# Kernel optimization log

Measured on AMD Instinct MI355X. Metric: run time of the kernel, lower is better.

Reference implementation:

```python
import jax, jax.numpy as jnp
import numpy as np

N = 8192       # batch size
BIT = 32       # hash code length
NCLASS = 100   # number of classes
ALPHA = 0.1    # config['alpha'] (quantization weight)
BEITA = 1.0    # config['beita'] (classification weight)
GAMMA = 0.1    # config['gamma'] (balancing weight)
P = 2          # config['p']


def setup_inputs() -> dict:
    key = jax.random.key(0)
    k1, k2, k3 = jax.random.split(key, 3)
    u = jax.random.normal(k1, (N, BIT), dtype=jnp.float32)
    Y = jax.random.normal(k2, (N, NCLASS), dtype=jnp.float32)
    labels = jax.random.randint(k3, (N,), 0, NCLASS)
    y = jax.nn.one_hot(labels, NCLASS, dtype=jnp.float32)  # one-hot targets
    return {"u": u, "Y": Y, "y": y}


def _hash_loss(u, y):
    n = u.shape[0]
    theta = (u @ u.T) * 0.5                       # [N, N]
    sim = (y @ y.T > 0).astype(u.dtype)           # [N, N] pairwise same-class
    # log(1 + exp(theta)) - Sim * theta  (logaddexp = stable same math)
    pair = jnp.logaddexp(0.0, theta) - sim * theta
    mask_pos = sim > 0
    s1 = sim.sum() - n                            # positives minus diagonal
    s0 = n * n - sim.sum()                        # negatives
    s0 = jnp.where(s0 == 0, 1.0, s0)
    s1 = jnp.where(s1 == 0, 1.0, s1)
    s = s0 + s1
    scale = jnp.where(mask_pos, s / s1, s / s0)
    pair = pair * scale
    # original subtracts diag of the *detached* rescaled matrix
    pair = pair - jax.lax.stop_gradient(jnp.diag(jnp.diag(pair)))
    count = n * (n - 1) / 2
    return pair.sum() / 2.0 / count


def reference(u, Y, y):
    likelihood_loss = _hash_loss(u, y)
    # CrossEntropyLoss with soft (one-hot float) targets
    logp = jax.nn.log_softmax(Y, axis=-1)
    classification_loss = -(y * logp).sum(axis=-1).mean()
    m = u.mean(axis=1)
    if P == 1:
        quantization_loss = ALPHA * jnp.abs(m).mean()
    else:
        quantization_loss = ALPHA * (m ** 2).mean()
    b = jnp.sign(u)
    balancing_loss = GAMMA * ((u - b) ** 2).mean()
    return likelihood_loss + BEITA * classification_loss + quantization_loss + balancing_loss
```

## Files before the change

kernel.cpp:

```cpp
#include <hip/hip_runtime.h>
#include <math.h>
#include <type_traits>

#define N 8192
#define BIT 32
#define NCLASS 100
#define ALPHA 0.1
#define BEITA 1.0
#define GAMMA 0.1

#define BT 128
#define NT (N / BT)
#define NPAIRBLK (NT * (NT + 1) / 2)
#define NPREP (N / 8)

#define SCALE_BF 0.84932181f
#define LN2 0.6931471805599453

typedef __attribute__((ext_vector_type(8))) short s16x8;
typedef __attribute__((ext_vector_type(4))) float f32x4;

#if __has_builtin(__builtin_amdgcn_exp2f)
static __device__ __forceinline__ float fexp2(float x) { return __builtin_amdgcn_exp2f(x); }
#else
static __device__ __forceinline__ float fexp2(float x) { return exp2f(x); }
#endif
#if __has_builtin(__builtin_amdgcn_logf)
static __device__ __forceinline__ float flog2(float x) { return __builtin_amdgcn_logf(x); }
#else
static __device__ __forceinline__ float flog2(float x) { return __log2f(x); }
#endif

static __device__ __forceinline__ unsigned short f2bf(float f) {
    unsigned int x = __float_as_uint(f);
    x += 0x7fff + ((x >> 16) & 1);
    return (unsigned short)(x >> 16);
}


__global__ __launch_bounds__(256) void prep_kernel(
    const float* __restrict__ u, const float* __restrict__ Y, const float* __restrict__ y,
    unsigned char* __restrict__ lab8, unsigned short* __restrict__ ubf,
    double* __restrict__ Pc, double* __restrict__ Pm, double* __restrict__ Pb)
{
    const int t = threadIdx.x;
    const int lane = t & 63;
    const int w = t >> 6;
    const int row0 = blockIdx.x * 8;

    float wcls = 0.f;
    #pragma unroll
    for (int rr = 0; rr < 2; ++rr) {
        const int r = row0 + w * 2 + rr;
        const float* Yp = Y + (size_t)r * NCLASS;
        const float* yp = y + (size_t)r * NCLASS;
        const bool has2 = lane < (NCLASS - 64);
        float Y0 = Yp[lane];
        float Y1 = has2 ? Yp[64 + lane] : -1e30f;
        float y0 = yp[lane];
        float y1 = has2 ? yp[64 + lane] : 0.f;
        float m = fmaxf(Y0, Y1);
        #pragma unroll
        for (int o = 32; o; o >>= 1) m = fmaxf(m, __shfl_xor(m, o, 64));
        float e  = __expf(Y0 - m) + (has2 ? __expf(Y1 - m) : 0.f);
        float tg = y0 * Y0 + (has2 ? y1 * Y1 : 0.f);
        #pragma unroll
        for (int o = 32; o; o >>= 1) { e += __shfl_xor(e, o, 64); tg += __shfl_xor(tg, o, 64); }
        unsigned long long b0 = __ballot(y0 > 0.5f);
        unsigned long long b1 = __ballot(has2 && (y1 > 0.5f));
        if (lane == 0) {
            int lbl = b0 ? (__ffsll((long long)b0) - 1) : (64 + __ffsll((long long)b1) - 1);
            lab8[r] = (unsigned char)lbl;
            wcls += m + __logf(e) - tg;
        }
    }

    const size_t uidx = (size_t)row0 * BIT + t;
    const float x = u[uidx];
    ubf[uidx] = f2bf(x * SCALE_BF);
    float bb = (x > 0.f) ? 1.f : ((x < 0.f) ? -1.f : 0.f);
    float d = x - bb;
    float bal = d * d;
    float rs = x;
    #pragma unroll
    for (int o = 1; o < 32; o <<= 1) rs += __shfl_xor(rs, o, 64);
    float mrow = rs * (1.f / BIT);
    float m2 = ((t & 31) == 0) ? mrow * mrow : 0.f;
    #pragma unroll
    for (int o = 32; o; o >>= 1) { m2 += __shfl_down(m2, o, 64); bal += __shfl_down(bal, o, 64); }

    __shared__ double red[4][3];
    if (lane == 0) { red[w][0] = (double)wcls; red[w][1] = (double)m2; red[w][2] = (double)bal; }
    __syncthreads();
    if (t == 0) {
        Pc[blockIdx.x] = red[0][0] + red[1][0] + red[2][0] + red[3][0];
        Pm[blockIdx.x] = red[0][1] + red[1][1] + red[2][1] + red[3][1];
        Pb[blockIdx.x] = red[0][2] + red[1][2] + red[2][2] + red[3][2];
    }
}

__global__ __launch_bounds__(256, 4) void pair_kernel(
    const unsigned short* __restrict__ ubf, const unsigned char* __restrict__ lab8,
    double* __restrict__ Ppos, double* __restrict__ Pneg)
{
    const int b = blockIdx.x;
    int ti = (int)(((float)(2 * NT + 1) - sqrtf((float)((2 * NT + 1) * (2 * NT + 1) - 8 * b))) * 0.5f);
    int S = ti * (2 * NT - ti + 1) / 2;
    if (S > b) { --ti; S = ti * (2 * NT - ti + 1) / 2; }
    else { int S2 = (ti + 1) * (2 * NT - ti) / 2; if (S2 <= b) { ++ti; S = S2; } }
    const int tj = ti + (b - S);
    const int i0 = ti * BT, j0 = tj * BT;

    const int t = threadIdx.x;
    const int lane = t & 63;
    const int w = t >> 6;
    const int wy = w >> 1, wx = w & 1;
    const int quad = lane >> 4, lr = lane & 15;
    const int ar = i0 + wy * 64;
    const int br = j0 + wx * 64;

    s16x8 av[4], bv[4];
    #pragma unroll
    for (int x = 0; x < 4; ++x) {
        av[x] = *(const s16x8*)(ubf + (size_t)(ar + x * 16 + lr) * BIT + quad * 8);
        bv[x] = *(const s16x8*)(ubf + (size_t)(br + x * 16 + lr) * BIT + quad * 8);
    }
    int lavp[4], lbv[4];
    #pragma unroll
    for (int a = 0; a < 4; ++a) lavp[a] = *(const int*)(lab8 + ar + a * 16 + quad * 4);
    #pragma unroll
    for (int c = 0; c < 4; ++c) lbv[c] = (int)lab8[br + c * 16 + lr];

    float sp0 = 0.f, sp1 = 0.f, sn0 = 0.f, sn1 = 0.f;
    auto run = [&](auto DIAGC) {
        constexpr bool DIAG = decltype(DIAGC)::value;
        #pragma unroll
        for (int a = 0; a < 4; ++a) {
            f32x4 acc[4];
            #pragma unroll
            for (int c = 0; c < 4; ++c)
                acc[c] = __builtin_amdgcn_mfma_f32_16x16x32_bf16(
                    av[a], bv[c], (f32x4){0.f, 0.f, 0.f, 0.f}, 0, 0, 0);

            #pragma unroll
            for (int r = 0; r < 4; ++r) {
                const int la = (lavp[a] >> (r * 8)) & 0xff;
                const int lrow = wy * 64 + a * 16 + quad * 4 + r;
                #pragma unroll
                for (int c = 0; c < 4; ++c) {
                    const float tv = acc[c][r];
                    float e  = fexp2(-fabsf(tv));
                    float l  = flog2(1.f + e);
                    float sl = fmaxf(tv, 0.f) + l;
                    float d  = sl - tv;
                    const bool sim = (la == lbv[c]);
                    float up = sim ? d : 0.f;
                    float un = sim ? 0.f : sl;
                    if (DIAG) {
                        const int lcol = wx * 64 + c * 16 + lr;
                        const bool keep = lcol > lrow;
                        up = keep ? up : 0.f;
                        un = keep ? un : 0.f;
                    }
                    if (r & 1) { sp1 += up; sn1 += un; }
                    else       { sp0 += up; sn0 += un; }
                }
            }
        }
    };
    if (ti == tj) run(std::integral_constant<bool, true>{});
    else          run(std::integral_constant<bool, false>{});

    float sp = sp0 + sp1, sn = sn0 + sn1;
    #pragma unroll
    for (int o = 32; o; o >>= 1) { sp += __shfl_down(sp, o, 64); sn += __shfl_down(sn, o, 64); }
    __shared__ float wredp[4], wredn[4];
    if (lane == 0) { wredp[w] = sp; wredn[w] = sn; }
    __syncthreads();
    if (t == 0) {
        Ppos[b] = (double)(wredp[0] + wredp[1] + wredp[2] + wredp[3]);
        Pneg[b] = (double)(wredn[0] + wredn[1] + wredn[2] + wredn[3]);
    }
}

__global__ __launch_bounds__(256) void fin_kernel(
    const unsigned char* __restrict__ lab8, const double* __restrict__ Ppos,
    const double* __restrict__ Pneg, const double* __restrict__ Pc,
    const double* __restrict__ Pm, const double* __restrict__ Pb, float* __restrict__ out)
{
    __shared__ int h[128];
    __shared__ double red[4][5];
    __shared__ double scd[2];
    const int t = threadIdx.x;
    const int lane = t & 63;
    const int w = t >> 6;

    if (t < 128) h[t] = 0;
    __syncthreads();
    #pragma unroll
    for (int k = 0; k < 32; ++k) atomicAdd(&h[lab8[t + k * 256]], 1);
    __syncthreads();

    if (w == 0) {
        long long c0 = (lane < NCLASS) ? h[lane] : 0;
        long long c1 = (lane + 64 < NCLASS) ? h[lane + 64] : 0;
        long long ss = c0 * c0 + c1 * c1;
        #pragma unroll
        for (int o = 32; o; o >>= 1) ss += __shfl_xor(ss, o, 64);
        if (lane == 0) {
            double s1 = (double)ss - (double)N;
            double s0 = (double)N * (double)N - (double)ss;
            if (s0 == 0.0) s0 = 1.0;
            if (s1 == 0.0) s1 = 1.0;
            double s = s0 + s1;
            scd[0] = (s / s1) * LN2;
            scd[1] = (s / s0) * LN2;
        }
    }

    double p0 = 0, p1 = 0, cc = 0, mm = 0, bb = 0;
    for (int i = t; i < NPAIRBLK; i += 256) { p0 += Ppos[i]; p1 += Pneg[i]; }
    for (int i = t; i < NPREP; i += 256)    { cc += Pc[i]; mm += Pm[i]; bb += Pb[i]; }
    #pragma unroll
    for (int o = 32; o; o >>= 1) {
        p0 += __shfl_down(p0, o, 64); p1 += __shfl_down(p1, o, 64);
        cc += __shfl_down(cc, o, 64); mm += __shfl_down(mm, o, 64);
        bb += __shfl_down(bb, o, 64);
    }
    if (lane == 0) { red[w][0] = p0; red[w][1] = p1; red[w][2] = cc; red[w][3] = mm; red[w][4] = bb; }
    __syncthreads();
    if (t == 0) {
        double a_pos = red[0][0] + red[1][0] + red[2][0] + red[3][0];
        double a_neg = red[0][1] + red[1][1] + red[2][1] + red[3][1];
        double a_cls = red[0][2] + red[1][2] + red[2][2] + red[3][2];
        double a_m2  = red[0][3] + red[1][3] + red[2][3] + red[3][3];
        double a_bal = red[0][4] + red[1][4] + red[2][4] + red[3][4];
        double pairsum = scd[0] * a_pos + scd[1] * a_neg;
        double lik   = 2.0 * pairsum / ((double)N * (double)(N - 1));
        double cls   = a_cls / (double)N;
        double quant = ALPHA * (a_m2 / (double)N);
        double bal   = GAMMA * (a_bal / ((double)N * (double)BIT));
        out[0] = (float)(lik + BEITA * cls + quant + bal);
    }
}

extern "C" void kernel_launch(void* const* d_in, const int* in_sizes, int n_in,
                              void* d_out, int out_size, void* d_ws, size_t ws_size,
                              hipStream_t stream) {
    const float* u = (const float*)d_in[0];
    const float* Y = (const float*)d_in[1];
    const float* y = (const float*)d_in[2];
    float* out = (float*)d_out;

    char* ws = (char*)d_ws;
    unsigned char*  lab8 = (unsigned char*)(ws + 1024);
    unsigned short* ubf  = (unsigned short*)(ws + 16384);
    double* Ppos = (double*)(ws + 557056);
    double* Pneg = (double*)(ws + 581632);
    double* Pc   = (double*)(ws + 606208);
    double* Pm   = (double*)(ws + 614400);
    double* Pb   = (double*)(ws + 622592);

    prep_kernel<<<NPREP, 256, 0, stream>>>(u, Y, y, lab8, ubf, Pc, Pm, Pb);
    pair_kernel<<<NPAIRBLK, 256, 0, stream>>>(ubf, lab8, Ppos, Pneg);
    fin_kernel<<<1, 256, 0, stream>>>(lab8, Ppos, Pneg, Pc, Pm, Pb, out);
}
```

Before: 92.46 us.

## Fuse final reduction into pair kernel via last-block counter; use 1024-thread blocks

```diff
diff --git a/kernel.cpp b/kernel.cpp
--- a/kernel.cpp
+++ b/kernel.cpp
@@ -41,12 +41,15 @@
 __global__ __launch_bounds__(256) void prep_kernel(
     const float* __restrict__ u, const float* __restrict__ Y, const float* __restrict__ y,
     unsigned char* __restrict__ lab8, unsigned short* __restrict__ ubf,
-    double* __restrict__ Pc, double* __restrict__ Pm, double* __restrict__ Pb)
+    double* __restrict__ Pc, double* __restrict__ Pm, double* __restrict__ Pb,
+    unsigned int* __restrict__ donecnt)
 {
     const int t = threadIdx.x;
     const int lane = t & 63;
     const int w = t >> 6;
     const int row0 = blockIdx.x * 8;
+
+    if (blockIdx.x == 0 && t == 0) *donecnt = 0;
 
     float wcls = 0.f;
     #pragma unroll
@@ -99,10 +102,19 @@
     }
 }
 
-__global__ __launch_bounds__(256, 4) void pair_kernel(
+__global__ __launch_bounds__(1024, 4) void pair_kernel(
     const unsigned short* __restrict__ ubf, const unsigned char* __restrict__ lab8,
-    double* __restrict__ Ppos, double* __restrict__ Pneg)
+    double* __restrict__ Ppos, double* __restrict__ Pneg,
+    const double* __restrict__ Pc, const double* __restrict__ Pm,
+    const double* __restrict__ Pb, unsigned int* __restrict__ donecnt,
+    float* __restrict__ out)
 {
+    __shared__ float wredp[16], wredn[16];
+    __shared__ int h[128];
+    __shared__ double redf[16][5];
+    __shared__ double scd[2];
+    __shared__ int amlast;
+
     const int b = blockIdx.x;
     int ti = (int)(((float)(2 * NT + 1) - sqrtf((float)((2 * NT + 1) * (2 * NT + 1) - 8 * b))) * 0.5f);
     int S = ti * (2 * NT - ti + 1) / 2;
@@ -114,41 +126,43 @@
     const int t = threadIdx.x;
     const int lane = t & 63;
     const int w = t >> 6;
-    const int wy = w >> 1, wx = w & 1;
+    const int wy = w >> 2, wx = w & 3;
     const int quad = lane >> 4, lr = lane & 15;
-    const int ar = i0 + wy * 64;
-    const int br = j0 + wx * 64;
-
-    s16x8 av[4], bv[4];
-    #pragma unroll
-    for (int x = 0; x < 4; ++x) {
+    const int ar = i0 + wy * 32;
+    const int br = j0 + wx * 32;
+
+    s16x8 av[2], bv[2];
+    #pragma unroll
+    for (int x = 0; x < 2; ++x) {
         av[x] = *(const s16x8*)(ubf + (size_t)(ar + x * 16 + lr) * BIT + quad * 8);
         bv[x] = *(const s16x8*)(ubf + (size_t)(br + x * 16 + lr) * BIT + quad * 8);
     }
-    int lavp[4], lbv[4];
-    #pragma unroll
-    for (int a = 0; a < 4; ++a) lavp[a] = *(const int*)(lab8 + ar + a * 16 + quad * 4);
-    #pragma unroll
-    for (int c = 0; c < 4; ++c) lbv[c] = (int)lab8[br + c * 16 + lr];
+    int lavp[2], lbv[2];
+    #pragma unroll
+    for (int a = 0; a < 2; ++a) lavp[a] = *(const int*)(lab8 + ar + a * 16 + quad * 4);
+    #pragma unroll
+    for (int c = 0; c < 2; ++c) lbv[c] = (int)lab8[br + c * 16 + lr];
 
     float sp0 = 0.f, sp1 = 0.f, sn0 = 0.f, sn1 = 0.f;
     auto run = [&](auto DIAGC) {
         constexpr bool DIAG = decltype(DIAGC)::value;
-        #pragma unroll
-        for (int a = 0; a < 4; ++a) {
-            f32x4 acc[4];
+        f32x4 acc[2][2];
+        #pragma unroll
+        for (int a = 0; a < 2; ++a)
             #pragma unroll
-            for (int c = 0; c < 4; ++c)
-                acc[c] = __builtin_amdgcn_mfma_f32_16x16x32_bf16(
+            for (int c = 0; c < 2; ++c)
+                acc[a][c] = __builtin_amdgcn_mfma_f32_16x16x32_bf16(
                     av[a], bv[c], (f32x4){0.f, 0.f, 0.f, 0.f}, 0, 0, 0);
 
+        #pragma unroll
+        for (int a = 0; a < 2; ++a) {
             #pragma unroll
             for (int r = 0; r < 4; ++r) {
                 const int la = (lavp[a] >> (r * 8)) & 0xff;
-                const int lrow = wy * 64 + a * 16 + quad * 4 + r;
+                const int lrow = wy * 32 + a * 16 + quad * 4 + r;
                 #pragma unroll
-                for (int c = 0; c < 4; ++c) {
-                    const float tv = acc[c][r];
+                for (int c = 0; c < 2; ++c) {
+                    const float tv = acc[a][c][r];
                     float e  = fexp2(-fabsf(tv));
                     float l  = flog2(1.f + e);
                     float sl = fmaxf(tv, 0.f) + l;
@@ -157,7 +171,7 @@
                     float up = sim ? d : 0.f;
                     float un = sim ? 0.f : sl;
                     if (DIAG) {
-                        const int lcol = wx * 64 + c * 16 + lr;
+                        const int lcol = wx * 32 + c * 16 + lr;
                         const bool keep = lcol > lrow;
                         up = keep ? up : 0.f;
                         un = keep ? un : 0.f;
@@ -174,31 +188,27 @@
     float sp = sp0 + sp1, sn = sn0 + sn1;
     #pragma unroll
     for (int o = 32; o; o >>= 1) { sp += __shfl_down(sp, o, 64); sn += __shfl_down(sn, o, 64); }
-    __shared__ float wredp[4], wredn[4];
     if (lane == 0) { wredp[w] = sp; wredn[w] = sn; }
     __syncthreads();
     if (t == 0) {
-        Ppos[b] = (double)(wredp[0] + wredp[1] + wredp[2] + wredp[3]);
-        Pneg[b] = (double)(wredn[0] + wredn[1] + wredn[2] + wredn[3]);
-    }
-}
-
-__global__ __launch_bounds__(256) void fin_kernel(
-    const unsigned char* __restrict__ lab8, const double* __restrict__ Ppos,
-    const double* __restrict__ Pneg, const double* __restrict__ Pc,
-    const double* __restrict__ Pm, const double* __restrict__ Pb, float* __restrict__ out)
-{
-    __shared__ int h[128];
-    __shared__ double red[4][5];
-    __shared__ double scd[2];
-    const int t = threadIdx.x;
-    const int lane = t & 63;
-    const int w = t >> 6;
+        double vp = 0.0, vn = 0.0;
+        #pragma unroll
+        for (int k = 0; k < 16; ++k) { vp += (double)wredp[k]; vn += (double)wredn[k]; }
+        Ppos[b] = vp;
+        Pneg[b] = vn;
+        __threadfence();
+        unsigned int old = atomicAdd(donecnt, 1u);
+        amlast = (old == (unsigned int)(NPAIRBLK - 1)) ? 1 : 0;
+    }
+    __syncthreads();
+    if (!amlast) return;
+
+    __threadfence();
 
     if (t < 128) h[t] = 0;
     __syncthreads();
     #pragma unroll
-    for (int k = 0; k < 32; ++k) atomicAdd(&h[lab8[t + k * 256]], 1);
+    for (int k = 0; k < 8; ++k) atomicAdd(&h[lab8[t + k * 1024]], 1);
     __syncthreads();
 
     if (w == 0) {
@@ -219,22 +229,23 @@
     }
 
     double p0 = 0, p1 = 0, cc = 0, mm = 0, bb = 0;
-    for (int i = t; i < NPAIRBLK; i += 256) { p0 += Ppos[i]; p1 += Pneg[i]; }
-    for (int i = t; i < NPREP; i += 256)    { cc += Pc[i]; mm += Pm[i]; bb += Pb[i]; }
+    for (int i = t; i < NPAIRBLK; i += 1024) { p0 += Ppos[i]; p1 += Pneg[i]; }
+    for (int i = t; i < NPREP; i += 1024)    { cc += Pc[i]; mm += Pm[i]; bb += Pb[i]; }
     #pragma unroll
     for (int o = 32; o; o >>= 1) {
         p0 += __shfl_down(p0, o, 64); p1 += __shfl_down(p1, o, 64);
         cc += __shfl_down(cc, o, 64); mm += __shfl_down(mm, o, 64);
         bb += __shfl_down(bb, o, 64);
     }
-    if (lane == 0) { red[w][0] = p0; red[w][1] = p1; red[w][2] = cc; red[w][3] = mm; red[w][4] = bb; }
+    if (lane == 0) { redf[w][0] = p0; redf[w][1] = p1; redf[w][2] = cc; redf[w][3] = mm; redf[w][4] = bb; }
     __syncthreads();
     if (t == 0) {
-        double a_pos = red[0][0] + red[1][0] + red[2][0] + red[3][0];
-        double a_neg = red[0][1] + red[1][1] + red[2][1] + red[3][1];
-        double a_cls = red[0][2] + red[1][2] + red[2][2] + red[3][2];
-        double a_m2  = red[0][3] + red[1][3] + red[2][3] + red[3][3];
-        double a_bal = red[0][4] + red[1][4] + red[2][4] + red[3][4];
+        double a_pos = 0, a_neg = 0, a_cls = 0, a_m2 = 0, a_bal = 0;
+        #pragma unroll
+        for (int k = 0; k < 16; ++k) {
+            a_pos += redf[k][0]; a_neg += redf[k][1]; a_cls += redf[k][2];
+            a_m2  += redf[k][3]; a_bal += redf[k][4];
+        }
         double pairsum = scd[0] * a_pos + scd[1] * a_neg;
         double lik   = 2.0 * pairsum / ((double)N * (double)(N - 1));
         double cls   = a_cls / (double)N;
@@ -253,6 +264,7 @@
     float* out = (float*)d_out;
 
     char* ws = (char*)d_ws;
+    unsigned int*   donecnt = (unsigned int*)(ws + 512);
     unsigned char*  lab8 = (unsigned char*)(ws + 1024);
     unsigned short* ubf  = (unsigned short*)(ws + 16384);
     double* Ppos = (double*)(ws + 557056);
@@ -261,7 +273,6 @@
     double* Pm   = (double*)(ws + 614400);
     double* Pb   = (double*)(ws + 622592);
 
-    prep_kernel<<<NPREP, 256, 0, stream>>>(u, Y, y, lab8, ubf, Pc, Pm, Pb);
-    pair_kernel<<<NPAIRBLK, 256, 0, stream>>>(ubf, lab8, Ppos, Pneg);
-    fin_kernel<<<1, 256, 0, stream>>>(lab8, Ppos, Pneg, Pc, Pm, Pb, out);
-}
+    prep_kernel<<<NPREP, 256, 0, stream>>>(u, Y, y, lab8, ubf, Pc, Pm, Pb, donecnt);
+    pair_kernel<<<NPAIRBLK, 1024, 0, stream>>>(ubf, lab8, Ppos, Pneg, Pc, Pm, Pb, donecnt, out);
+}
```

Result: slower. 114.4 us (+23.7%).

## Fuse final reduction into pair kernel and simplify softplus evaluation

Applied to the files above, without the earlier changes.

```diff
diff --git a/kernel.cpp b/kernel.cpp
--- a/kernel.cpp
+++ b/kernel.cpp
@@ -41,12 +41,15 @@
 __global__ __launch_bounds__(256) void prep_kernel(
     const float* __restrict__ u, const float* __restrict__ Y, const float* __restrict__ y,
     unsigned char* __restrict__ lab8, unsigned short* __restrict__ ubf,
-    double* __restrict__ Pc, double* __restrict__ Pm, double* __restrict__ Pb)
+    double* __restrict__ Pc, double* __restrict__ Pm, double* __restrict__ Pb,
+    unsigned int* __restrict__ donecnt)
 {
     const int t = threadIdx.x;
     const int lane = t & 63;
     const int w = t >> 6;
     const int row0 = blockIdx.x * 8;
+
+    if (blockIdx.x == 0 && t == 0) *donecnt = 0;
 
     float wcls = 0.f;
     #pragma unroll
@@ -99,10 +102,19 @@
     }
 }
 
-__global__ __launch_bounds__(256, 4) void pair_kernel(
+__global__ __launch_bounds__(256, 6) void pair_kernel(
     const unsigned short* __restrict__ ubf, const unsigned char* __restrict__ lab8,
-    double* __restrict__ Ppos, double* __restrict__ Pneg)
+    double* __restrict__ Ppos, double* __restrict__ Pneg,
+    const double* __restrict__ Pc, const double* __restrict__ Pm,
+    const double* __restrict__ Pb, unsigned int* __restrict__ donecnt,
+    float* __restrict__ out)
 {
+    __shared__ float wredp[4], wredn[4];
+    __shared__ int h[128];
+    __shared__ double redf[4][5];
+    __shared__ double scd[2];
+    __shared__ int amlast;
+
     const int b = blockIdx.x;
     int ti = (int)(((float)(2 * NT + 1) - sqrtf((float)((2 * NT + 1) * (2 * NT + 1) - 8 * b))) * 0.5f);
     int S = ti * (2 * NT - ti + 1) / 2;
@@ -149,9 +161,7 @@
                 #pragma unroll
                 for (int c = 0; c < 4; ++c) {
                     const float tv = acc[c][r];
-                    float e  = fexp2(-fabsf(tv));
-                    float l  = flog2(1.f + e);
-                    float sl = fmaxf(tv, 0.f) + l;
+                    float sl = flog2(1.f + fexp2(tv));
                     float d  = sl - tv;
                     const bool sim = (la == lbv[c]);
                     float up = sim ? d : 0.f;
@@ -174,26 +184,21 @@
     float sp = sp0 + sp1, sn = sn0 + sn1;
     #pragma unroll
     for (int o = 32; o; o >>= 1) { sp += __shfl_down(sp, o, 64); sn += __shfl_down(sn, o, 64); }
-    __shared__ float wredp[4], wredn[4];
     if (lane == 0) { wredp[w] = sp; wredn[w] = sn; }
     __syncthreads();
     if (t == 0) {
-        Ppos[b] = (double)(wredp[0] + wredp[1] + wredp[2] + wredp[3]);
-        Pneg[b] = (double)(wredn[0] + wredn[1] + wredn[2] + wredn[3]);
-    }
-}
-
-__global__ __launch_bounds__(256) void fin_kernel(
-    const unsigned char* __restrict__ lab8, const double* __restrict__ Ppos,
-    const double* __restrict__ Pneg, const double* __restrict__ Pc,
-    const double* __restrict__ Pm, const double* __restrict__ Pb, float* __restrict__ out)
-{
-    __shared__ int h[128];
-    __shared__ double red[4][5];
-    __shared__ double scd[2];
-    const int t = threadIdx.x;
-    const int lane = t & 63;
-    const int w = t >> 6;
+        double vp = (double)wredp[0] + (double)wredp[1] + (double)wredp[2] + (double)wredp[3];
+        double vn = (double)wredn[0] + (double)wredn[1] + (double)wredn[2] + (double)wredn[3];
+        Ppos[b] = vp;
+        Pneg[b] = vn;
+        __threadfence();
+        unsigned int old = atomicAdd(donecnt, 1u);
+        amlast = (old == (unsigned int)(NPAIRBLK - 1)) ? 1 : 0;
+    }
+    __syncthreads();
+    if (!amlast) return;
+
+    __threadfence();
 
     if (t < 128) h[t] = 0;
     __syncthreads();
@@ -227,14 +232,14 @@
         cc += __shfl_down(cc, o, 64); mm += __shfl_down(mm, o, 64);
         bb += __shfl_down(bb, o, 64);
     }
-    if (lane == 0) { red[w][0] = p0; red[w][1] = p1; red[w][2] = cc; red[w][3] = mm; red[w][4] = bb; }
+    if (lane == 0) { redf[w][0] = p0; redf[w][1] = p1; redf[w][2] = cc; redf[w][3] = mm; redf[w][4] = bb; }
     __syncthreads();
     if (t == 0) {
-        double a_pos = red[0][0] + red[1][0] + red[2][0] + red[3][0];
-        double a_neg = red[0][1] + red[1][1] + red[2][1] + red[3][1];
-        double a_cls = red[0][2] + red[1][2] + red[2][2] + red[3][2];
-        double a_m2  = red[0][3] + red[1][3] + red[2][3] + red[3][3];
-        double a_bal = red[0][4] + red[1][4] + red[2][4] + red[3][4];
+        double a_pos = redf[0][0] + redf[1][0] + redf[2][0] + redf[3][0];
+        double a_neg = redf[0][1] + redf[1][1] + redf[2][1] + redf[3][1];
+        double a_cls = redf[0][2] + redf[1][2] + redf[2][2] + redf[3][2];
+        double a_m2  = redf[0][3] + redf[1][3] + redf[2][3] + redf[3][3];
+        double a_bal = redf[0][4] + redf[1][4] + redf[2][4] + redf[3][4];
         double pairsum = scd[0] * a_pos + scd[1] * a_neg;
         double lik   = 2.0 * pairsum / ((double)N * (double)(N - 1));
         double cls   = a_cls / (double)N;
@@ -253,6 +258,7 @@
     float* out = (float*)d_out;
 
     char* ws = (char*)d_ws;
+    unsigned int*   donecnt = (unsigned int*)(ws + 512);
     unsigned char*  lab8 = (unsigned char*)(ws + 1024);
     unsigned short* ubf  = (unsigned short*)(ws + 16384);
     double* Ppos = (double*)(ws + 557056);
@@ -261,7 +267,6 @@
     double* Pm   = (double*)(ws + 614400);
     double* Pb   = (double*)(ws + 622592);
 
-    prep_kernel<<<NPREP, 256, 0, stream>>>(u, Y, y, lab8, ubf, Pc, Pm, Pb);
-    pair_kernel<<<NPAIRBLK, 256, 0, stream>>>(ubf, lab8, Ppos, Pneg);
-    fin_kernel<<<1, 256, 0, stream>>>(lab8, Ppos, Pneg, Pc, Pm, Pb, out);
-}
+    prep_kernel<<<NPREP, 256, 0, stream>>>(u, Y, y, lab8, ubf, Pc, Pm, Pb, donecnt);
+    pair_kernel<<<NPAIRBLK, 256, 0, stream>>>(ubf, lab8, Ppos, Pneg, Pc, Pm, Pb, donecnt, out);
+}
```

Result: slower. 117.2 us (+26.8%).
